# Performance work log

Hardware: AMD Instinct MI355X
Metric: run time of the kernel (lower is better)

## Reference

```python
import jax, jax.numpy as jnp
import numpy as np

EMBED_DIM = 512
NUM_HEADS = 8
HEAD_DIM = EMBED_DIM // NUM_HEADS
N = 4096
E = 131072
EPS = 1e-5
NEG = -1e9


def layer_norm(x, g, b):
    mu = jnp.mean(x, axis=-1, keepdims=True)
    var = jnp.mean(jnp.square(x - mu), axis=-1, keepdims=True)
    return (x - mu) * jax.lax.rsqrt(var + EPS) * g + b


def setup_inputs() -> dict:
    key = jax.random.key(0)
    ks = jax.random.split(key, 12)
    D = EMBED_DIM
    s = 1.0 / np.sqrt(D)
    return {
        "x": jax.random.normal(ks[0], (N, D), jnp.float32),
        "edge_index": jax.random.randint(ks[1], (2, E), 0, N, jnp.int64),
        "edge_weight": jax.random.uniform(ks[2], (E,), jnp.float32),
        "Wqkv": jax.random.normal(ks[3], (3 * D, D), jnp.float32) * s,
        "bqkv": jnp.zeros((3 * D,), jnp.float32),
        "Wo": jax.random.normal(ks[4], (D, D), jnp.float32) * s,
        "bo": jnp.zeros((D,), jnp.float32),
        "W1": jax.random.normal(ks[5], (D, D), jnp.float32) * s,
        "b1": jnp.zeros((D,), jnp.float32),
        "g1": jnp.ones((D,), jnp.float32),
        "beta1": jnp.zeros((D,), jnp.float32),
        "g2": jnp.ones((D,), jnp.float32),
        "beta2": jnp.zeros((D,), jnp.float32),
    }


def reference(x, edge_index, edge_weight, Wqkv, bqkv, Wo, bo, W1, b1, g1, beta1, g2, beta2):
    n = x.shape[0]
    # dense NxN additive bias: -1e9 everywhere, 0 on diagonal, edge weights at (dst, src)
    src, dst = edge_index[0], edge_index[1]
    diag = jnp.arange(n)
    bias = jnp.full((n, n), NEG, dtype=x.dtype)
    bias = bias.at[diag, diag].set(0.0)
    bias = bias.at[dst, src].set(edge_weight.astype(x.dtype))

    # multi-head self-attention (torch nn.MultiheadAttention semantics)
    qkv = x @ Wqkv.T + bqkv                       # (N, 3D)
    q, k, v = jnp.split(qkv, 3, axis=-1)          # each (N, D)
    q = q.reshape(n, NUM_HEADS, HEAD_DIM).transpose(1, 0, 2)  # (H, N, hd)
    k = k.reshape(n, NUM_HEADS, HEAD_DIM).transpose(1, 0, 2)
    v = v.reshape(n, NUM_HEADS, HEAD_DIM).transpose(1, 0, 2)
    scores = jnp.einsum("hnd,hmd->hnm", q, k) / np.sqrt(HEAD_DIM)  # (H, N, N)
    scores = scores + bias[None, :, :]
    attn = jax.nn.softmax(scores, axis=-1)
    out = jnp.einsum("hnm,hmd->hnd", attn, v)     # (H, N, hd)
    out = out.transpose(1, 0, 2).reshape(n, EMBED_DIM)
    attn_out = out @ Wo.T + bo

    # residual + LN + FFN (single linear, no activation) + residual + LN
    h = layer_norm(x + attn_out, g1, beta1)
    h = layer_norm(h + (h @ W1.T + b1), g2, beta2)
    return h
```

## Files before the change

### kernel.cpp

```cpp
#include <hip/hip_runtime.h>

#define NNODES 4096
#define DIM 512
#define QKVD 1536
#define MAXE 96

typedef __bf16 bf16_t;
typedef bf16_t bf16x8 __attribute__((ext_vector_type(8)));
typedef bf16_t bf16x2 __attribute__((ext_vector_type(2)));
typedef float f32x4 __attribute__((ext_vector_type(4)));
typedef unsigned int uint;

__global__ __launch_bounds__(256) void cast_all_k(const float* __restrict__ x,
                                                  const float* __restrict__ wqkv,
                                                  const float* __restrict__ wo,
                                                  const float* __restrict__ w1,
                                                  bf16_t* __restrict__ xb,
                                                  bf16_t* __restrict__ wqkvb,
                                                  bf16_t* __restrict__ wob,
                                                  bf16_t* __restrict__ w1b,
                                                  uint* __restrict__ deg) {
  int i = blockIdx.x * 256 + threadIdx.x;
  if (blockIdx.x < 16) deg[i] = 0u;
  const float* src;
  bf16_t* dst;
  int off;
  if (i < 524288) { src = x; dst = xb; off = i; }
  else if (i < 720896) { src = wqkv; dst = wqkvb; off = i - 524288; }
  else if (i < 786432) { src = wo; dst = wob; off = i - 720896; }
  else { src = w1; dst = w1b; off = i - 786432; }
  float4 v = ((const float4*)src)[off];
  dst[4 * off + 0] = (bf16_t)v.x;
  dst[4 * off + 1] = (bf16_t)v.y;
  dst[4 * off + 2] = (bf16_t)v.z;
  dst[4 * off + 3] = (bf16_t)v.w;
}

__global__ __launch_bounds__(256) void fill_bucket_k(const int* __restrict__ ei,
                                                     uint* __restrict__ deg,
                                                     int* __restrict__ colv,
                                                     uint* __restrict__ eidv, int E) {
  int e = blockIdx.x * 256 + threadIdx.x;
  if (e < E) {
    int src = ei[e] & (NNODES - 1);
    int dst = ei[E + e] & (NNODES - 1);
    uint pos = atomicAdd(&deg[dst], 1u);
    if (pos < MAXE) {
      colv[dst * MAXE + pos] = src;
      eidv[dst * MAXE + pos] = (uint)e + 1u;
    }
  }
}

template <bool OUT_BF16>
__global__ __launch_bounds__(256) void gemm_bt(const bf16_t* __restrict__ A,
                                               const bf16_t* __restrict__ B,
                                               const float* __restrict__ bias,
                                               void* __restrict__ Cout,
                                               int M, int Nt, int K) {
  __shared__ bf16_t As[128][40];
  __shared__ bf16_t Bs[64][40];
  const int t = threadIdx.x;
  const int lane = t & 63, w = t >> 6;
  const int wr = (w >> 1) * 64, wc = (w & 1) * 32;
  const int m0 = blockIdx.y * 128, n0 = blockIdx.x * 64;
  f32x4 acc[4][2] = {};
  const int r_ld = t >> 2;
  const int c_ld = (t & 3) * 8;

  for (int k0 = 0; k0 < K; k0 += 32) {
    *(int4*)&As[r_ld][c_ld] = *(const int4*)(A + (long)(m0 + r_ld) * K + k0 + c_ld);
    *(int4*)&As[r_ld + 64][c_ld] = *(const int4*)(A + (long)(m0 + r_ld + 64) * K + k0 + c_ld);
    *(int4*)&Bs[r_ld][c_ld] = *(const int4*)(B + (long)(n0 + r_ld) * K + k0 + c_ld);
    __syncthreads();
    bf16x8 af[4], bfr[2];
    const int kg = (lane >> 4) * 8;
#pragma unroll
    for (int i = 0; i < 4; ++i)
      af[i] = *(const bf16x8*)&As[wr + i * 16 + (lane & 15)][kg];
#pragma unroll
    for (int j = 0; j < 2; ++j)
      bfr[j] = *(const bf16x8*)&Bs[wc + j * 16 + (lane & 15)][kg];
#pragma unroll
    for (int i = 0; i < 4; ++i)
#pragma unroll
      for (int j = 0; j < 2; ++j)
        acc[i][j] = __builtin_amdgcn_mfma_f32_16x16x32_bf16(af[i], bfr[j], acc[i][j], 0, 0, 0);
    __syncthreads();
  }

  const int cr = (lane >> 4) * 4;
  const int cc = lane & 15;
#pragma unroll
  for (int i = 0; i < 4; ++i) {
#pragma unroll
    for (int j = 0; j < 2; ++j) {
      int n = n0 + wc + j * 16 + cc;
      float bv = bias[n];
#pragma unroll
      for (int r = 0; r < 4; ++r) {
        int m = m0 + wr + i * 16 + cr + r;
        float vv = acc[i][j][r] + bv;
        if (OUT_BF16)
          ((bf16_t*)Cout)[(long)m * Nt + n] = (bf16_t)vv;
        else
          ((float*)Cout)[(long)m * Nt + n] = vv;
      }
    }
  }
}

__global__ __launch_bounds__(512) void attn_fused_k(const bf16_t* __restrict__ qkv,
                                                    const float* __restrict__ ew,
                                                    const uint* __restrict__ deg,
                                                    const int* __restrict__ colv,
                                                    const uint* __restrict__ eidv,
                                                    bf16_t* __restrict__ outb) {
  __shared__ float scs[8][MAXE + 1];
  __shared__ int srcs[MAXE + 1];
  __shared__ uint eids[MAXE + 1];
  __shared__ int vld[MAXE + 1];
  __shared__ float invs_s[8];
  __shared__ float vacc[8][DIM];

  const int i = blockIdx.x;
  const int t = threadIdx.x;
  const int lane = t & 63, w = t >> 6;

  uint dg = deg[i];
  int L = (dg < (uint)MAXE) ? (int)dg : MAXE;
  int n = L + 1;

  if (t < L) {
    srcs[t] = colv[i * MAXE + t];
    eids[t] = eidv[i * MAXE + t];
  }
  if (t == L) { srcs[L] = i; eids[L] = 0u; }
  __syncthreads();

  const bf16x8 qv = *(const bf16x8*)(qkv + (long)i * QKVD + lane * 8);
  int val[8], ec[8];
#pragma unroll
  for (int u = 0; u < 8; ++u) {
    int ee = w + 8 * u;
    val[u] = ee < n;
    ec[u] = val[u] ? ee : 0;
  }
  bf16x8 kpre[8], vpre[8];
#pragma unroll
  for (int u = 0; u < 8; ++u) {
    long rb = (long)srcs[ec[u]] * QKVD;
    kpre[u] = *(const bf16x8*)(qkv + rb + DIM + lane * 8);
    vpre[u] = *(const bf16x8*)(qkv + rb + 2 * DIM + lane * 8);
  }
  float bpre[8];
#pragma unroll
  for (int u = 0; u < 8; ++u) {
    uint id = eids[ec[u]];
    bpre[u] = (id == 0u) ? 0.f : ew[id - 1u];
  }

  if (t < n) {
    int sj = srcs[t];
    uint my = eids[t];
    int ok = 1;
    for (int j = 0; j < n; ++j)
      ok &= !((srcs[j] == sj) & (eids[j] > my));
    vld[t] = ok;
  }
  __syncthreads();

#pragma unroll
  for (int u = 0; u < 8; ++u) {
    float d = 0.f;
#pragma unroll
    for (int j = 0; j < 8; ++j) d += (float)qv[j] * (float)kpre[u][j];
#pragma unroll
    for (int o = 1; o < 8; o <<= 1) d += __shfl_xor(d, o);
    if (((lane & 7) == 0) & val[u]) {
      int e = w + 8 * u;
      scs[lane >> 3][e] = vld[e] ? (d * 0.125f + bpre[u]) : -1e30f;
    }
  }
  for (int e = w + 64; e < n; e += 8) {
    const bf16x8 ka = *(const bf16x8*)(qkv + (long)srcs[e] * QKVD + DIM + lane * 8);
    float d = 0.f;
#pragma unroll
    for (int j = 0; j < 8; ++j) d += (float)qv[j] * (float)ka[j];
#pragma unroll
    for (int o = 1; o < 8; o <<= 1) d += __shfl_xor(d, o);
    if ((lane & 7) == 0) {
      uint id = eids[e];
      float b = (id == 0u) ? 0.f : ew[id - 1u];
      scs[lane >> 3][e] = vld[e] ? (d * 0.125f + b) : -1e30f;
    }
  }
  __syncthreads();

  {
    float m = -1e30f;
    for (int e = lane; e < n; e += 64) m = fmaxf(m, scs[w][e]);
#pragma unroll
    for (int o = 32; o > 0; o >>= 1) m = fmaxf(m, __shfl_xor(m, o));
    float ps = 0.f;
    for (int e = lane; e < n; e += 64) {
      float ev = __expf(scs[w][e] - m);
      scs[w][e] = ev;
      ps += ev;
    }
#pragma unroll
    for (int o = 32; o > 0; o >>= 1) ps += __shfl_xor(ps, o);
    if (lane == 0) invs_s[w] = 1.f / ps;
  }
  __syncthreads();

  const int hl = lane >> 3;
  float a8[8] = {0.f, 0.f, 0.f, 0.f, 0.f, 0.f, 0.f, 0.f};
#pragma unroll
  for (int u = 0; u < 8; ++u) {
    float p = val[u] ? scs[hl][w + 8 * u] : 0.f;
#pragma unroll
    for (int j = 0; j < 8; ++j) a8[j] += p * (float)vpre[u][j];
  }
  for (int e = w + 64; e < n; e += 8) {
    const bf16x8 vv = *(const bf16x8*)(qkv + (long)srcs[e] * QKVD + 2 * DIM + lane * 8);
    float p = scs[hl][e];
#pragma unroll
    for (int j = 0; j < 8; ++j) a8[j] += p * (float)vv[j];
  }
#pragma unroll
  for (int j = 0; j < 8; ++j) vacc[w][lane * 8 + j] = a8[j];
  __syncthreads();

  {
    float s = 0.f;
#pragma unroll
    for (int ww = 0; ww < 8; ++ww) s += vacc[ww][t];
    outb[(long)i * DIM + t] = (bf16_t)(s * invs_s[t >> 6]);
  }
}

__global__ __launch_bounds__(64) void ln_k(const float* __restrict__ a,
                                           const float* __restrict__ b,
                                           const float* __restrict__ g,
                                           const float* __restrict__ beta,
                                           float* __restrict__ of,
                                           bf16_t* __restrict__ ob) {
  const int row = blockIdx.x;
  const int l = threadIdx.x;
  const float* pa = a + (long)row * DIM;
  const float* pb = b + (long)row * DIM;
  float v[8];
  float s = 0.f;
#pragma unroll
  for (int j = 0; j < 8; ++j) {
    int d = l + j * 64;
    v[j] = pa[d] + pb[d];
    s += v[j];
  }
#pragma unroll
  for (int o = 32; o > 0; o >>= 1) s += __shfl_xor(s, o);
  float mu = s * (1.f / 512.f);
  float q = 0.f;
#pragma unroll
  for (int j = 0; j < 8; ++j) {
    float dd = v[j] - mu;
    q += dd * dd;
  }
#pragma unroll
  for (int o = 32; o > 0; o >>= 1) q += __shfl_xor(q, o);
  float inv = rsqrtf(q * (1.f / 512.f) + 1e-5f);
#pragma unroll
  for (int j = 0; j < 8; ++j) {
    int d = l + j * 64;
    float y = (v[j] - mu) * inv * g[d] + beta[d];
    of[(long)row * DIM + d] = y;
    if (ob) ob[(long)row * DIM + d] = (bf16_t)y;
  }
}

extern "C" void kernel_launch(void* const* d_in, const int* in_sizes, int n_in,
                              void* d_out, int out_size, void* d_ws, size_t ws_size,
                              hipStream_t stream) {
  const float* x = (const float*)d_in[0];
  const int* ei = (const int*)d_in[1];
  const float* ew = (const float*)d_in[2];
  const float* Wqkv = (const float*)d_in[3];
  const float* bqkv = (const float*)d_in[4];
  const float* Wo = (const float*)d_in[5];
  const float* bo = (const float*)d_in[6];
  const float* W1 = (const float*)d_in[7];
  const float* b1 = (const float*)d_in[8];
  const float* g1 = (const float*)d_in[9];
  const float* be1 = (const float*)d_in[10];
  const float* g2 = (const float*)d_in[11];
  const float* be2 = (const float*)d_in[12];
  float* out = (float*)d_out;
  const int E = in_sizes[1] / 2;

  char* ws = (char*)d_ws;
  bf16_t* qkvb = (bf16_t*)(ws + 0);
  bf16_t* xb = (bf16_t*)(ws + 12582912);
  bf16_t* Wqkvb = (bf16_t*)(ws + 16777216);
  bf16_t* Wob = (bf16_t*)(ws + 18350080);
  bf16_t* W1b = (bf16_t*)(ws + 18874368);
  bf16_t* outb = (bf16_t*)(ws + 19398656);
  float* h = (float*)(ws + 23592960);
  bf16_t* hb = (bf16_t*)(ws + 31981568);
  float* f = (float*)(ws + 36175872);
  uint* deg = (uint*)(ws + 23592960);
  int* colv = (int*)(ws + 23609344);
  uint* eidv = (uint*)(ws + 25182208);
  float* attn_out = (float*)(ws + 0);

  cast_all_k<<<3328, 256, 0, stream>>>(x, Wqkv, Wo, W1, xb, Wqkvb, Wob, W1b, deg);
  fill_bucket_k<<<(E + 255) / 256, 256, 0, stream>>>(ei, deg, colv, eidv, E);

  gemm_bt<true><<<dim3(QKVD / 64, NNODES / 128), 256, 0, stream>>>(
      xb, Wqkvb, bqkv, (void*)qkvb, NNODES, QKVD, DIM);

  attn_fused_k<<<NNODES, 512, 0, stream>>>(qkvb, ew, deg, colv, eidv, outb);

  gemm_bt<false><<<dim3(DIM / 64, NNODES / 128), 256, 0, stream>>>(
      outb, Wob, bo, (void*)attn_out, NNODES, DIM, DIM);

  ln_k<<<NNODES, 64, 0, stream>>>(x, attn_out, g1, be1, h, hb);

  gemm_bt<false><<<dim3(DIM / 64, NNODES / 128), 256, 0, stream>>>(
      hb, W1b, b1, (void*)f, NNODES, DIM, DIM);

  ln_k<<<NNODES, 64, 0, stream>>>(h, f, g2, be2, out, nullptr);
}
```

Before: 129.6 us.

## Stage attention K/V rows in LDS via direct loads; widen QKV GEMM tile

```diff
diff --git a/kernel.cpp b/kernel.cpp
--- a/kernel.cpp
+++ b/kernel.cpp
@@ -4,12 +4,17 @@
 #define DIM 512
 #define QKVD 1536
 #define MAXE 96
+#define STAGE 56
 
 typedef __bf16 bf16_t;
 typedef bf16_t bf16x8 __attribute__((ext_vector_type(8)));
 typedef bf16_t bf16x2 __attribute__((ext_vector_type(2)));
 typedef float f32x4 __attribute__((ext_vector_type(4)));
 typedef unsigned int uint;
+
+#define GLOAD_LDS16(gp, lp)                                                        \
+  __builtin_amdgcn_global_load_lds((const __attribute__((address_space(1))) void*)(gp), \
+                                   (__attribute__((address_space(3))) void*)(lp), 16, 0, 0)
 
 __global__ __launch_bounds__(256) void cast_all_k(const float* __restrict__ x,
                                                   const float* __restrict__ wqkv,
@@ -52,6 +57,61 @@
   }
 }
 
+__global__ __launch_bounds__(256) void gemm128_bt(const bf16_t* __restrict__ A,
+                                                  const bf16_t* __restrict__ B,
+                                                  const float* __restrict__ bias,
+                                                  bf16_t* __restrict__ Cout,
+                                                  int M, int Nt, int K) {
+  __shared__ bf16_t As[128][40];
+  __shared__ bf16_t Bs[128][40];
+  const int t = threadIdx.x;
+  const int lane = t & 63, w = t >> 6;
+  const int wr = (w >> 1) * 64, wc = (w & 1) * 64;
+  const int m0 = blockIdx.y * 128, n0 = blockIdx.x * 128;
+  f32x4 acc[4][4] = {};
+  const int r_ld = t >> 2;
+  const int c_ld = (t & 3) * 8;
+
+  for (int k0 = 0; k0 < K; k0 += 32) {
+#pragma unroll
+    for (int seg = 0; seg < 2; ++seg) {
+      int row = r_ld + seg * 64;
+      *(int4*)&As[row][c_ld] = *(const int4*)(A + (long)(m0 + row) * K + k0 + c_ld);
+      *(int4*)&Bs[row][c_ld] = *(const int4*)(B + (long)(n0 + row) * K + k0 + c_ld);
+    }
+    __syncthreads();
+    bf16x8 af[4], bfr[4];
+    const int kg = (lane >> 4) * 8;
+#pragma unroll
+    for (int i = 0; i < 4; ++i) {
+      af[i] = *(const bf16x8*)&As[wr + i * 16 + (lane & 15)][kg];
+      bfr[i] = *(const bf16x8*)&Bs[wc + i * 16 + (lane & 15)][kg];
+    }
+#pragma unroll
+    for (int i = 0; i < 4; ++i)
+#pragma unroll
+      for (int j = 0; j < 4; ++j)
+        acc[i][j] = __builtin_amdgcn_mfma_f32_16x16x32_bf16(af[i], bfr[j], acc[i][j], 0, 0, 0);
+    __syncthreads();
+  }
+
+  const int cr = (lane >> 4) * 4;
+  const int cc = lane & 15;
+#pragma unroll
+  for (int i = 0; i < 4; ++i) {
+#pragma unroll
+    for (int j = 0; j < 4; ++j) {
+      int n = n0 + wc + j * 16 + cc;
+      float bv = bias[n];
+#pragma unroll
+      for (int r = 0; r < 4; ++r) {
+        int m = m0 + wr + i * 16 + cr + r;
+        Cout[(long)m * Nt + n] = (bf16_t)(acc[i][j][r] + bv);
+      }
+    }
+  }
+}
+
 template <bool OUT_BF16>
 __global__ __launch_bounds__(256) void gemm_bt(const bf16_t* __restrict__ A,
                                                const bf16_t* __restrict__ B,
@@ -110,18 +170,18 @@
   }
 }
 
-__global__ __launch_bounds__(512) void attn_fused_k(const bf16_t* __restrict__ qkv,
+__global__ __launch_bounds__(512) void attn_stage_k(const bf16_t* __restrict__ qkv,
                                                     const float* __restrict__ ew,
                                                     const uint* __restrict__ deg,
                                                     const int* __restrict__ colv,
                                                     const uint* __restrict__ eidv,
                                                     bf16_t* __restrict__ outb) {
+  __shared__ __align__(16) bf16_t kvs[STAGE][DIM];
   __shared__ float scs[8][MAXE + 1];
   __shared__ int srcs[MAXE + 1];
   __shared__ uint eids[MAXE + 1];
   __shared__ int vld[MAXE + 1];
   __shared__ float invs_s[8];
-  __shared__ float vacc[8][DIM];
 
   const int i = blockIdx.x;
   const int t = threadIdx.x;
@@ -130,6 +190,7 @@
   uint dg = deg[i];
   int L = (dg < (uint)MAXE) ? (int)dg : MAXE;
   int n = L + 1;
+  int ns = (n < STAGE) ? n : STAGE;
 
   if (t < L) {
     srcs[t] = colv[i * MAXE + t];
@@ -138,27 +199,10 @@
   if (t == L) { srcs[L] = i; eids[L] = 0u; }
   __syncthreads();
 
+  for (int e = w; e < ns; e += 8)
+    GLOAD_LDS16(qkv + (long)srcs[e] * QKVD + DIM + lane * 8, &kvs[e][0]);
+
   const bf16x8 qv = *(const bf16x8*)(qkv + (long)i * QKVD + lane * 8);
-  int val[8], ec[8];
-#pragma unroll
-  for (int u = 0; u < 8; ++u) {
-    int ee = w + 8 * u;
-    val[u] = ee < n;
-    ec[u] = val[u] ? ee : 0;
-  }
-  bf16x8 kpre[8], vpre[8];
-#pragma unroll
-  for (int u = 0; u < 8; ++u) {
-    long rb = (long)srcs[ec[u]] * QKVD;
-    kpre[u] = *(const bf16x8*)(qkv + rb + DIM + lane * 8);
-    vpre[u] = *(const bf16x8*)(qkv + rb + 2 * DIM + lane * 8);
-  }
-  float bpre[8];
-#pragma unroll
-  for (int u = 0; u < 8; ++u) {
-    uint id = eids[ec[u]];
-    bpre[u] = (id == 0u) ? 0.f : ew[id - 1u];
-  }
 
   if (t < n) {
     int sj = srcs[t];
@@ -170,23 +214,11 @@
   }
   __syncthreads();
 
-#pragma unroll
-  for (int u = 0; u < 8; ++u) {
+  for (int e = w; e < ns; e += 8) {
+    const bf16x8 kr = *(const bf16x8*)&kvs[e][lane * 8];
     float d = 0.f;
 #pragma unroll
-    for (int j = 0; j < 8; ++j) d += (float)qv[j] * (float)kpre[u][j];
-#pragma unroll
-    for (int o = 1; o < 8; o <<= 1) d += __shfl_xor(d, o);
-    if (((lane & 7) == 0) & val[u]) {
-      int e = w + 8 * u;
-      scs[lane >> 3][e] = vld[e] ? (d * 0.125f + bpre[u]) : -1e30f;
-    }
-  }
-  for (int e = w + 64; e < n; e += 8) {
-    const bf16x8 ka = *(const bf16x8*)(qkv + (long)srcs[e] * QKVD + DIM + lane * 8);
-    float d = 0.f;
-#pragma unroll
-    for (int j = 0; j < 8; ++j) d += (float)qv[j] * (float)ka[j];
+    for (int j = 0; j < 8; ++j) d += (float)qv[j] * (float)kr[j];
 #pragma unroll
     for (int o = 1; o < 8; o <<= 1) d += __shfl_xor(d, o);
     if ((lane & 7) == 0) {
@@ -195,7 +227,23 @@
       scs[lane >> 3][e] = vld[e] ? (d * 0.125f + b) : -1e30f;
     }
   }
-  __syncthreads();
+  for (int e = STAGE + w; e < n; e += 8) {
+    const bf16x8 ka = *(const bf16x8*)(qkv + (long)srcs[e] * QKVD + DIM + lane * 8);
+    float d = 0.f;
+#pragma unroll
+    for (int j = 0; j < 8; ++j) d += (float)qv[j] * (float)ka[j];
+#pragma unroll
+    for (int o = 1; o < 8; o <<= 1) d += __shfl_xor(d, o);
+    if ((lane & 7) == 0) {
+      uint id = eids[e];
+      float b = (id == 0u) ? 0.f : ew[id - 1u];
+      scs[lane >> 3][e] = vld[e] ? (d * 0.125f + b) : -1e30f;
+    }
+  }
+  __syncthreads();
+
+  for (int e = w; e < ns; e += 8)
+    GLOAD_LDS16(qkv + (long)srcs[e] * QKVD + 2 * DIM + lane * 8, &kvs[e][0]);
 
   {
     float m = -1e30f;
@@ -216,26 +264,28 @@
 
   const int hl = lane >> 3;
   float a8[8] = {0.f, 0.f, 0.f, 0.f, 0.f, 0.f, 0.f, 0.f};
-#pragma unroll
-  for (int u = 0; u < 8; ++u) {
-    float p = val[u] ? scs[hl][w + 8 * u] : 0.f;
-#pragma unroll
-    for (int j = 0; j < 8; ++j) a8[j] += p * (float)vpre[u][j];
-  }
-  for (int e = w + 64; e < n; e += 8) {
+  for (int e = w; e < ns; e += 8) {
+    const bf16x8 vr = *(const bf16x8*)&kvs[e][lane * 8];
+    float p = scs[hl][e];
+#pragma unroll
+    for (int j = 0; j < 8; ++j) a8[j] += p * (float)vr[j];
+  }
+  for (int e = STAGE + w; e < n; e += 8) {
     const bf16x8 vv = *(const bf16x8*)(qkv + (long)srcs[e] * QKVD + 2 * DIM + lane * 8);
     float p = scs[hl][e];
 #pragma unroll
     for (int j = 0; j < 8; ++j) a8[j] += p * (float)vv[j];
   }
-#pragma unroll
-  for (int j = 0; j < 8; ++j) vacc[w][lane * 8 + j] = a8[j];
-  __syncthreads();
-
+  __syncthreads();
+
+  float* vacc = (float*)&kvs[0][0];
+#pragma unroll
+  for (int j = 0; j < 8; ++j) vacc[w * DIM + lane * 8 + j] = a8[j];
+  __syncthreads();
   {
     float s = 0.f;
 #pragma unroll
-    for (int ww = 0; ww < 8; ++ww) s += vacc[ww][t];
+    for (int ww = 0; ww < 8; ++ww) s += vacc[ww * DIM + t];
     outb[(long)i * DIM + t] = (bf16_t)(s * invs_s[t >> 6]);
   }
 }
@@ -316,10 +366,10 @@
   cast_all_k<<<3328, 256, 0, stream>>>(x, Wqkv, Wo, W1, xb, Wqkvb, Wob, W1b, deg);
   fill_bucket_k<<<(E + 255) / 256, 256, 0, stream>>>(ei, deg, colv, eidv, E);
 
-  gemm_bt<true><<<dim3(QKVD / 64, NNODES / 128), 256, 0, stream>>>(
-      xb, Wqkvb, bqkv, (void*)qkvb, NNODES, QKVD, DIM);
-
-  attn_fused_k<<<NNODES, 512, 0, stream>>>(qkvb, ew, deg, colv, eidv, outb);
+  gemm128_bt<<<dim3(QKVD / 128, NNODES / 128), 256, 0, stream>>>(
+      xb, Wqkvb, bqkv, qkvb, NNODES, QKVD, DIM);
+
+  attn_stage_k<<<NNODES, 512, 0, stream>>>(qkvb, ew, deg, colv, eidv, outb);
 
   gemm_bt<false><<<dim3(DIM / 64, NNODES / 128), 256, 0, stream>>>(
       outb, Wob, bo, (void*)attn_out, NNODES, DIM, DIM);
```

Measured after the change: 140.8 us. +8.6%, slower.
